# Kernel tuning notes

Hardware: AMD Instinct MI355X
Metric: run time of the kernel (lower is better)

## Reference

```python
import jax, jax.numpy as jnp
import numpy as np

B, H, W, C = 32, 64, 64, 256


def setup_inputs() -> dict:
    key = jax.random.key(0)
    ks = jax.random.split(key, 4)
    scale = 1.0 / np.sqrt(C)
    return {
        "x": jax.random.normal(ks[0], (B, H, W, C), dtype=jnp.float32),
        "wq": jax.random.normal(ks[1], (C, C), dtype=jnp.float32) * scale,
        "bq": jnp.zeros((C,), dtype=jnp.float32),
        "wk": jax.random.normal(ks[2], (C, C), dtype=jnp.float32) * scale,
        "bk": jnp.zeros((C,), dtype=jnp.float32),
        "wv": jax.random.normal(ks[3], (C, C), dtype=jnp.float32) * scale,
        "bv": jnp.zeros((C,), dtype=jnp.float32),
    }


def reference(x, wq, bq, wk, bk, wv, bv):
    # 1x1 convs == per-pixel dense projections
    q = jnp.einsum('bhwc,cf->bhwf', x, wq) + bq
    k = jnp.einsum('bhwc,cf->bhwf', x, wk) + bk
    v = jnp.einsum('bhwc,cf->bhwf', x, wv) + bv
    # tf.matmul(key, query, transpose_b=True): batch dims (b,h), contract over c
    attn = jnp.einsum('bhwc,bhvc->bhwv', k, q)  # [B,H,W,W], NO 1/sqrt(d) scaling
    attn = jax.nn.softmax(attn, axis=-1)
    out = jnp.einsum('bhwv,bhvc->bhwc', attn, v)  # [B,H,W,C]
    return out * x  # elementwise gate with raw input
```

## Files before the change

### kernel.cpp

```cpp
#include <hip/hip_runtime.h>

#define CD   256
#define WD   64
#define NBH  2048
#define XST  264
#define VST  72
#define SST  68

typedef unsigned short u16;
typedef __attribute__((ext_vector_type(8))) short bfrag_t;
typedef __attribute__((ext_vector_type(4))) float f4_t;

#define MFMA(a, b, c) __builtin_amdgcn_mfma_f32_16x16x32_bf16(a, b, c, 0, 0, 0)

__device__ __forceinline__ u16 f2bf(float f) {
    unsigned u = __float_as_uint(f);
    u += 0x7fffu + ((u >> 16) & 1u);
    return (u16)(u >> 16);
}
__device__ __forceinline__ float bf2f(u16 h) {
    return __uint_as_float(((unsigned)h) << 16);
}

__global__ __launch_bounds__(256) void prep_m(
    const float* __restrict__ wq, const float* __restrict__ wk,
    u16* __restrict__ Mthi, u16* __restrict__ Mtlo)
{
    __shared__ float swq[16 * 257];
    __shared__ float swk[32 * 257];
    const int t = threadIdx.x;
    const int dt = blockIdx.x >> 3;
    const int ct = blockIdx.x & 7;
    #pragma unroll
    for (int n = 0; n < 16; ++n) {
        int idx = n * 256 + t;
        int d = idx >> 8, f = idx & 255;
        swq[d * 257 + f] = wq[(dt * 16 + d) * CD + f];
    }
    #pragma unroll
    for (int n = 0; n < 32; ++n) {
        int idx = n * 256 + t;
        int c = idx >> 8, f = idx & 255;
        swk[c * 257 + f] = wk[(ct * 32 + c) * CD + f];
    }
    __syncthreads();
    const int d = t & 15, c0 = (t >> 4) * 2;
    #pragma unroll
    for (int cc = 0; cc < 2; ++cc) {
        const float* kr = &swk[(c0 + cc) * 257];
        const float* qr = &swq[d * 257];
        float acc = 0.f;
        #pragma unroll 8
        for (int f = 0; f < CD; ++f) acc = fmaf(kr[f], qr[f], acc);
        u16 h = f2bf(acc);
        int off = (dt * 16 + d) * CD + ct * 32 + c0 + cc;
        Mthi[off] = h;
        Mtlo[off] = f2bf(acc - bf2f(h));
    }
}

__global__ __launch_bounds__(256) void prep_v(
    const float* __restrict__ wv, u16* __restrict__ Wvthi)
{
    __shared__ float tile[64 * 65];
    const int t = threadIdx.x;
    const int bc = blockIdx.x >> 2, bd = blockIdx.x & 3;
    #pragma unroll
    for (int n = 0; n < 16; ++n) {
        int idx = n * 256 + t;
        int c = idx >> 6, d = idx & 63;
        tile[c * 65 + d] = wv[(bc * 64 + c) * CD + bd * 64 + d];
    }
    __syncthreads();
    #pragma unroll
    for (int n = 0; n < 16; ++n) {
        int idx = n * 256 + t;
        int d = idx >> 6, c = idx & 63;
        Wvthi[(bd * 64 + d) * CD + bc * 64 + c] = f2bf(tile[c * 65 + d]);
    }
}

__global__ __launch_bounds__(256) void prep_b(
    const float* __restrict__ wq, const float* __restrict__ bk,
    float* __restrict__ wqbk)
{
    __shared__ float sbk[CD];
    const int t = threadIdx.x;
    if (t < CD) sbk[t] = bk[t];
    __syncthreads();
    const int c = blockIdx.x * 16 + (t >> 4), part = t & 15;
    const float* wr = wq + c * CD + part * 16;
    const float* br = sbk + part * 16;
    float a = 0.f;
    #pragma unroll
    for (int j = 0; j < 16; ++j) a = fmaf(wr[j], br[j], a);
    a += __shfl_xor(a, 1);
    a += __shfl_xor(a, 2);
    a += __shfl_xor(a, 4);
    a += __shfl_xor(a, 8);
    if (part == 0) wqbk[c] = a;
}

extern __shared__ char smem_raw[];

__global__ __launch_bounds__(1024, 4) void attn_kernel(
    const float* __restrict__ x,
    const u16* __restrict__ Mthi, const u16* __restrict__ Mtlo,
    const u16* __restrict__ Wvthi, const float* __restrict__ wqbk,
    const float* __restrict__ bv, float* __restrict__ out)
{
    u16* sXhi = (u16*)smem_raw;
    u16* sXlo = sXhi + WD * XST;
    u16* sThi = sXlo + WD * XST;
    u16* sTlo = sThi + WD * XST;
    u16* sVt  = sThi;
    float* sS  = (float*)(sTlo + WD * XST);
    float* sxb = sS + WD * SST;
    float* sbv = sxb + WD;

    const int t = threadIdx.x;
    const int wave = t >> 6, lane = t & 63;
    const int lane15 = lane & 15, quad = lane >> 4;
    const int bh = blockIdx.x;
    const float* __restrict__ xblk = x + (size_t)bh * (WD * CD);
    float* __restrict__ oblk = out + (size_t)bh * (WD * CD);

    if (t < CD) sbv[t] = bv[t];
    {
        const float4* xv4 = (const float4*)xblk;
        #pragma unroll
        for (int n = 0; n < 4; ++n) {
            int idx = n * 1024 + t;
            float4 v = xv4[idx];
            int i = idx >> 6;
            int c = (idx & 63) << 2;
            ushort4 h4, l4;
            h4.x = f2bf(v.x); l4.x = f2bf(v.x - bf2f(h4.x));
            h4.y = f2bf(v.y); l4.y = f2bf(v.y - bf2f(h4.y));
            h4.z = f2bf(v.z); l4.z = f2bf(v.z - bf2f(h4.z));
            h4.w = f2bf(v.w); l4.w = f2bf(v.w - bf2f(h4.w));
            *(ushort4*)&sXhi[i * XST + c] = h4;
            *(ushort4*)&sXlo[i * XST + c] = l4;
        }
    }
    {
        const int row = t >> 4, part = t & 15;
        const float* xr = xblk + row * CD + part * 16;
        const float* br = wqbk + part * 16;
        float a = 0.f;
        #pragma unroll
        for (int i = 0; i < 4; ++i) {
            float4 xv = *(const float4*)&xr[i * 4];
            float4 bvv = *(const float4*)&br[i * 4];
            a = fmaf(xv.x, bvv.x, a); a = fmaf(xv.y, bvv.y, a);
            a = fmaf(xv.z, bvv.z, a); a = fmaf(xv.w, bvv.w, a);
        }
        a += __shfl_xor(a, 1);
        a += __shfl_xor(a, 2);
        a += __shfl_xor(a, 4);
        a += __shfl_xor(a, 8);
        if (part == 0) sxb[row] = a;
    }
    __syncthreads();

    {
        f4_t acc[4];
        const f4_t z = {0.f, 0.f, 0.f, 0.f};
        #pragma unroll
        for (int a = 0; a < 4; ++a) acc[a] = z;

        const int drow = wave * 16 + lane15;
        #pragma unroll
        for (int kk = 0; kk < 8; ++kk) {
            const int k0 = kk * 32 + quad * 8;
            const int mo = drow * CD + k0;
            bfrag_t Ah = *(const bfrag_t*)(Mthi + mo);
            bfrag_t Al = *(const bfrag_t*)(Mtlo + mo);
            bfrag_t Bh[4], Bl[4];
            #pragma unroll
            for (int nt = 0; nt < 4; ++nt) {
                const int xo = (nt * 16 + lane15) * XST + k0;
                Bh[nt] = *(const bfrag_t*)(sXhi + xo);
                Bl[nt] = *(const bfrag_t*)(sXlo + xo);
            }
            #pragma unroll
            for (int nt = 0; nt < 4; ++nt) {
                acc[nt] = MFMA(Ah, Bh[nt], acc[nt]);
                acc[nt] = MFMA(Ah, Bl[nt], acc[nt]);
                acc[nt] = MFMA(Al, Bh[nt], acc[nt]);
            }
        }
        #pragma unroll
        for (int nt = 0; nt < 4; ++nt) {
            const int i  = nt * 16 + lane15;
            const int d0 = wave * 16 + quad * 4;
            ushort4 h4, l4;
            float f;
            f = acc[nt][0]; h4.x = f2bf(f); l4.x = f2bf(f - bf2f(h4.x));
            f = acc[nt][1]; h4.y = f2bf(f); l4.y = f2bf(f - bf2f(h4.y));
            f = acc[nt][2]; h4.z = f2bf(f); l4.z = f2bf(f - bf2f(h4.z));
            f = acc[nt][3]; h4.w = f2bf(f); l4.w = f2bf(f - bf2f(h4.w));
            *(ushort4*)&sThi[i * XST + d0] = h4;
            *(ushort4*)&sTlo[i * XST + d0] = l4;
        }
    }
    __syncthreads();

    {
        f4_t acc = {0.f, 0.f, 0.f, 0.f};
        const int m0 = (wave >> 2) * 16;
        const int n0 = (wave & 3) * 16;
        #pragma unroll
        for (int kk = 0; kk < 8; ++kk) {
            const int k0 = kk * 32 + quad * 8;
            const int to = (m0 + lane15) * XST + k0;
            const int xo = (n0 + lane15) * XST + k0;
            bfrag_t Th = *(const bfrag_t*)(sThi + to);
            bfrag_t Tl = *(const bfrag_t*)(sTlo + to);
            bfrag_t Xh = *(const bfrag_t*)(sXhi + xo);
            bfrag_t Xl = *(const bfrag_t*)(sXlo + xo);
            acc = MFMA(Th, Xh, acc);
            acc = MFMA(Th, Xl, acc);
            acc = MFMA(Tl, Xh, acc);
        }
        const int v = n0 + lane15;
        const float xbv = sxb[v];
        #pragma unroll
        for (int r = 0; r < 4; ++r) {
            const int wtok = m0 + quad * 4 + r;
            sS[wtok * SST + v] = acc[r] + xbv;
        }
    }
    __syncthreads();

    {
        f4_t acc[4];
        const f4_t z = {0.f, 0.f, 0.f, 0.f};
        #pragma unroll
        for (int a = 0; a < 4; ++a) acc[a] = z;

        const int drow = wave * 16 + lane15;
        #pragma unroll
        for (int kk = 0; kk < 8; ++kk) {
            const int k0 = kk * 32 + quad * 8;
            bfrag_t Af = *(const bfrag_t*)(Wvthi + drow * CD + k0);
            #pragma unroll
            for (int nt = 0; nt < 4; ++nt) {
                bfrag_t Bf = *(const bfrag_t*)(sXhi + (nt * 16 + lane15) * XST + k0);
                acc[nt] = MFMA(Af, Bf, acc[nt]);
            }
        }
        #pragma unroll
        for (int nt = 0; nt < 4; ++nt) {
            const int j = nt * 16 + lane15;
            #pragma unroll
            for (int r = 0; r < 4; ++r) {
                const int d = wave * 16 + quad * 4 + r;
                sVt[d * VST + j] = f2bf(acc[nt][r] + sbv[d]);
            }
        }
    }
    {
        const int row = t >> 4, part = t & 15;
        float* srow = &sS[row * SST + part * 4];
        float e[4];
        float mx = fmaxf(fmaxf(srow[0], srow[1]), fmaxf(srow[2], srow[3]));
        mx = fmaxf(mx, __shfl_xor(mx, 1));
        mx = fmaxf(mx, __shfl_xor(mx, 2));
        mx = fmaxf(mx, __shfl_xor(mx, 4));
        mx = fmaxf(mx, __shfl_xor(mx, 8));
        float sum = 0.f;
        #pragma unroll
        for (int u = 0; u < 4; ++u) { e[u] = __expf(srow[u] - mx); sum += e[u]; }
        sum += __shfl_xor(sum, 1);
        sum += __shfl_xor(sum, 2);
        sum += __shfl_xor(sum, 4);
        sum += __shfl_xor(sum, 8);
        float inv = 1.0f / sum;
        #pragma unroll
        for (int u = 0; u < 4; ++u) srow[u] = e[u] * inv;
    }
    __syncthreads();

    {
        f4_t acc[4];
        const f4_t z = {0.f, 0.f, 0.f, 0.f};
        #pragma unroll
        for (int a = 0; a < 4; ++a) acc[a] = z;

        const int m0 = (wave & 3) * 16;
        const int nbase = (wave >> 2) * 64;
        #pragma unroll
        for (int kk = 0; kk < 2; ++kk) {
            const int k0 = kk * 32 + quad * 8;
            const float* p = &sS[(m0 + lane15) * SST + k0];
            f4_t p0 = *(const f4_t*)p;
            f4_t p1 = *(const f4_t*)(p + 4);
            bfrag_t Af;
            Af[0] = (short)f2bf(p0[0]); Af[1] = (short)f2bf(p0[1]);
            Af[2] = (short)f2bf(p0[2]); Af[3] = (short)f2bf(p0[3]);
            Af[4] = (short)f2bf(p1[0]); Af[5] = (short)f2bf(p1[1]);
            Af[6] = (short)f2bf(p1[2]); Af[7] = (short)f2bf(p1[3]);
            #pragma unroll
            for (int nt = 0; nt < 4; ++nt) {
                bfrag_t Bf = *(const bfrag_t*)(sVt + (nbase + nt * 16 + lane15) * VST + k0);
                acc[nt] = MFMA(Af, Bf, acc[nt]);
            }
        }
        #pragma unroll
        for (int nt = 0; nt < 4; ++nt) {
            const int d = nbase + nt * 16 + lane15;
            #pragma unroll
            for (int r = 0; r < 4; ++r) {
                const int wtok = m0 + quad * 4 + r;
                float g = xblk[wtok * CD + d];
                oblk[wtok * CD + d] = acc[nt][r] * g;
            }
        }
    }
}

extern "C" void kernel_launch(void* const* d_in, const int* in_sizes, int n_in,
                              void* d_out, int out_size, void* d_ws, size_t ws_size,
                              hipStream_t stream) {
    const float* x  = (const float*)d_in[0];
    const float* wq = (const float*)d_in[1];
    const float* wk = (const float*)d_in[3];
    const float* bk = (const float*)d_in[4];
    const float* wv = (const float*)d_in[5];
    const float* bv = (const float*)d_in[6];
    float* out = (float*)d_out;

    char* ws = (char*)d_ws;
    u16* Mthi   = (u16*)ws;
    u16* Mtlo   = (u16*)(ws + (128 << 10));
    u16* Wvthi  = (u16*)(ws + (256 << 10));
    float* wqbk = (float*)(ws + (384 << 10));

    prep_m<<<128, 256, 0, stream>>>(wq, wk, Mthi, Mtlo);
    prep_v<<<16, 256, 0, stream>>>(wv, Wvthi);
    prep_b<<<16, 256, 0, stream>>>(wq, bk, wqbk);

    const size_t lds = (size_t)(4 * WD * XST * sizeof(u16)) +
                       (WD * SST + WD + CD) * sizeof(float);
    hipFuncSetAttribute((const void*)attn_kernel,
                        hipFuncAttributeMaxDynamicSharedMemorySize, (int)lds);
    attn_kernel<<<NBH, 1024, lds, stream>>>(x, Mthi, Mtlo, Wvthi, wqbk, bv, out);
}
```

Before: 374.6 us.

## Merge prep kernels, preload weight fragments, split MFMA accumulator chains

Fuses the three weight-preparation kernels into one launch, with block index ranges selecting each task, to cut launch overhead. In the attention kernel, all global weight fragments (Mthi/Mtlo and Wvthi) are loaded into registers up front, so global latency is exposed once rather than inside the MFMA loop. The score GEMM now uses three independent accumulators instead of one serial chain of dependent MFMAs. Costs are higher register pressure under a 1024-thread launch bound and a slightly different float summation order.

Measured after the change: 374.3 us. Within noise of the previous version (-0.1%).

```diff
diff --git a/kernel.cpp b/kernel.cpp
--- a/kernel.cpp
+++ b/kernel.cpp
@@ -22,83 +22,80 @@
     return __uint_as_float(((unsigned)h) << 16);
 }
 
-__global__ __launch_bounds__(256) void prep_m(
+__global__ __launch_bounds__(256) void prep_all(
     const float* __restrict__ wq, const float* __restrict__ wk,
-    u16* __restrict__ Mthi, u16* __restrict__ Mtlo)
+    const float* __restrict__ wv, const float* __restrict__ bk,
+    u16* __restrict__ Mthi, u16* __restrict__ Mtlo,
+    u16* __restrict__ Wvthi, float* __restrict__ wqbk)
 {
-    __shared__ float swq[16 * 257];
-    __shared__ float swk[32 * 257];
+    __shared__ float smem[12336];
     const int t = threadIdx.x;
-    const int dt = blockIdx.x >> 3;
-    const int ct = blockIdx.x & 7;
-    #pragma unroll
-    for (int n = 0; n < 16; ++n) {
-        int idx = n * 256 + t;
-        int d = idx >> 8, f = idx & 255;
-        swq[d * 257 + f] = wq[(dt * 16 + d) * CD + f];
-    }
-    #pragma unroll
-    for (int n = 0; n < 32; ++n) {
-        int idx = n * 256 + t;
-        int c = idx >> 8, f = idx & 255;
-        swk[c * 257 + f] = wk[(ct * 32 + c) * CD + f];
-    }
-    __syncthreads();
-    const int d = t & 15, c0 = (t >> 4) * 2;
-    #pragma unroll
-    for (int cc = 0; cc < 2; ++cc) {
-        const float* kr = &swk[(c0 + cc) * 257];
-        const float* qr = &swq[d * 257];
-        float acc = 0.f;
-        #pragma unroll 8
-        for (int f = 0; f < CD; ++f) acc = fmaf(kr[f], qr[f], acc);
-        u16 h = f2bf(acc);
-        int off = (dt * 16 + d) * CD + ct * 32 + c0 + cc;
-        Mthi[off] = h;
-        Mtlo[off] = f2bf(acc - bf2f(h));
-    }
-}
-
-__global__ __launch_bounds__(256) void prep_v(
-    const float* __restrict__ wv, u16* __restrict__ Wvthi)
-{
-    __shared__ float tile[64 * 65];
-    const int t = threadIdx.x;
-    const int bc = blockIdx.x >> 2, bd = blockIdx.x & 3;
-    #pragma unroll
-    for (int n = 0; n < 16; ++n) {
-        int idx = n * 256 + t;
-        int c = idx >> 6, d = idx & 63;
-        tile[c * 65 + d] = wv[(bc * 64 + c) * CD + bd * 64 + d];
-    }
-    __syncthreads();
-    #pragma unroll
-    for (int n = 0; n < 16; ++n) {
-        int idx = n * 256 + t;
-        int d = idx >> 6, c = idx & 63;
-        Wvthi[(bd * 64 + d) * CD + bc * 64 + c] = f2bf(tile[c * 65 + d]);
-    }
-}
-
-__global__ __launch_bounds__(256) void prep_b(
-    const float* __restrict__ wq, const float* __restrict__ bk,
-    float* __restrict__ wqbk)
-{
-    __shared__ float sbk[CD];
-    const int t = threadIdx.x;
-    if (t < CD) sbk[t] = bk[t];
-    __syncthreads();
-    const int c = blockIdx.x * 16 + (t >> 4), part = t & 15;
-    const float* wr = wq + c * CD + part * 16;
-    const float* br = sbk + part * 16;
-    float a = 0.f;
-    #pragma unroll
-    for (int j = 0; j < 16; ++j) a = fmaf(wr[j], br[j], a);
-    a += __shfl_xor(a, 1);
-    a += __shfl_xor(a, 2);
-    a += __shfl_xor(a, 4);
-    a += __shfl_xor(a, 8);
-    if (part == 0) wqbk[c] = a;
+    const int b = blockIdx.x;
+
+    if (b < 128) {
+        float* swq = smem;
+        float* swk = smem + 16 * 257;
+        const int dt = b >> 3;
+        const int ct = b & 7;
+        #pragma unroll
+        for (int n = 0; n < 16; ++n) {
+            int idx = n * 256 + t;
+            int d = idx >> 8, f = idx & 255;
+            swq[d * 257 + f] = wq[(dt * 16 + d) * CD + f];
+        }
+        #pragma unroll
+        for (int n = 0; n < 32; ++n) {
+            int idx = n * 256 + t;
+            int c = idx >> 8, f = idx & 255;
+            swk[c * 257 + f] = wk[(ct * 32 + c) * CD + f];
+        }
+        __syncthreads();
+        const int d = t & 15, c0 = (t >> 4) * 2;
+        #pragma unroll
+        for (int cc = 0; cc < 2; ++cc) {
+            const float* kr = &swk[(c0 + cc) * 257];
+            const float* qr = &swq[d * 257];
+            float acc = 0.f;
+            #pragma unroll 8
+            for (int f = 0; f < CD; ++f) acc = fmaf(kr[f], qr[f], acc);
+            u16 h = f2bf(acc);
+            int off = (dt * 16 + d) * CD + ct * 32 + c0 + cc;
+            Mthi[off] = h;
+            Mtlo[off] = f2bf(acc - bf2f(h));
+        }
+    } else if (b < 144) {
+        float* tile = smem;
+        const int bb = b - 128;
+        const int bc = bb >> 2, bd = bb & 3;
+        #pragma unroll
+        for (int n = 0; n < 16; ++n) {
+            int idx = n * 256 + t;
+            int c = idx >> 6, d = idx & 63;
+            tile[c * 65 + d] = wv[(bc * 64 + c) * CD + bd * 64 + d];
+        }
+        __syncthreads();
+        #pragma unroll
+        for (int n = 0; n < 16; ++n) {
+            int idx = n * 256 + t;
+            int d = idx >> 6, c = idx & 63;
+            Wvthi[(bd * 64 + d) * CD + bc * 64 + c] = f2bf(tile[c * 65 + d]);
+        }
+    } else {
+        float* sbk = smem;
+        if (t < CD) sbk[t] = bk[t];
+        __syncthreads();
+        const int c = (b - 144) * 16 + (t >> 4), part = t & 15;
+        const float* wr = wq + c * CD + part * 16;
+        const float* br = sbk + part * 16;
+        float a = 0.f;
+        #pragma unroll
+        for (int j = 0; j < 16; ++j) a = fmaf(wr[j], br[j], a);
+        a += __shfl_xor(a, 1);
+        a += __shfl_xor(a, 2);
+        a += __shfl_xor(a, 4);
+        a += __shfl_xor(a, 8);
+        if (part == 0) wqbk[c] = a;
+    }
 }
 
 extern __shared__ char smem_raw[];
@@ -170,12 +167,17 @@
         for (int a = 0; a < 4; ++a) acc[a] = z;
 
         const int drow = wave * 16 + lane15;
+        const u16* mh = Mthi + drow * CD + quad * 8;
+        const u16* ml = Mtlo + drow * CD + quad * 8;
+        bfrag_t Ah[8], Al[8];
+        #pragma unroll
+        for (int kk = 0; kk < 8; ++kk) {
+            Ah[kk] = *(const bfrag_t*)(mh + kk * 32);
+            Al[kk] = *(const bfrag_t*)(ml + kk * 32);
+        }
         #pragma unroll
         for (int kk = 0; kk < 8; ++kk) {
             const int k0 = kk * 32 + quad * 8;
-            const int mo = drow * CD + k0;
-            bfrag_t Ah = *(const bfrag_t*)(Mthi + mo);
-            bfrag_t Al = *(const bfrag_t*)(Mtlo + mo);
             bfrag_t Bh[4], Bl[4];
             #pragma unroll
             for (int nt = 0; nt < 4; ++nt) {
@@ -185,9 +187,9 @@
             }
             #pragma unroll
             for (int nt = 0; nt < 4; ++nt) {
-                acc[nt] = MFMA(Ah, Bh[nt], acc[nt]);
-                acc[nt] = MFMA(Ah, Bl[nt], acc[nt]);
-                acc[nt] = MFMA(Al, Bh[nt], acc[nt]);
+                acc[nt] = MFMA(Ah[kk], Bh[nt], acc[nt]);
+                acc[nt] = MFMA(Ah[kk], Bl[nt], acc[nt]);
+                acc[nt] = MFMA(Al[kk], Bh[nt], acc[nt]);
             }
         }
         #pragma unroll
@@ -207,7 +209,8 @@
     __syncthreads();
 
     {
-        f4_t acc = {0.f, 0.f, 0.f, 0.f};
+        const f4_t z = {0.f, 0.f, 0.f, 0.f};
+        f4_t a0 = z, a1 = z, a2 = z;
         const int m0 = (wave >> 2) * 16;
         const int n0 = (wave & 3) * 16;
         #pragma unroll
@@ -219,16 +222,16 @@
             bfrag_t Tl = *(const bfrag_t*)(sTlo + to);
             bfrag_t Xh = *(const bfrag_t*)(sXhi + xo);
             bfrag_t Xl = *(const bfrag_t*)(sXlo + xo);
-            acc = MFMA(Th, Xh, acc);
-            acc = MFMA(Th, Xl, acc);
-            acc = MFMA(Tl, Xh, acc);
+            a0 = MFMA(Th, Xh, a0);
+            a1 = MFMA(Th, Xl, a1);
+            a2 = MFMA(Tl, Xh, a2);
         }
         const int v = n0 + lane15;
         const float xbv = sxb[v];
         #pragma unroll
         for (int r = 0; r < 4; ++r) {
             const int wtok = m0 + quad * 4 + r;
-            sS[wtok * SST + v] = acc[r] + xbv;
+            sS[wtok * SST + v] = a0[r] + a1[r] + a2[r] + xbv;
         }
     }
     __syncthreads();
@@ -240,14 +243,18 @@
         for (int a = 0; a < 4; ++a) acc[a] = z;
 
         const int drow = wave * 16 + lane15;
+        const u16* wvp = Wvthi + drow * CD + quad * 8;
+        bfrag_t Av[8];
+        #pragma unroll
+        for (int kk = 0; kk < 8; ++kk)
+            Av[kk] = *(const bfrag_t*)(wvp + kk * 32);
         #pragma unroll
         for (int kk = 0; kk < 8; ++kk) {
             const int k0 = kk * 32 + quad * 8;
-            bfrag_t Af = *(const bfrag_t*)(Wvthi + drow * CD + k0);
             #pragma unroll
             for (int nt = 0; nt < 4; ++nt) {
                 bfrag_t Bf = *(const bfrag_t*)(sXhi + (nt * 16 + lane15) * XST + k0);
-                acc[nt] = MFMA(Af, Bf, acc[nt]);
+                acc[nt] = MFMA(Av[kk], Bf, acc[nt]);
             }
         }
         #pragma unroll
@@ -337,9 +344,7 @@
     u16* Wvthi  = (u16*)(ws + (256 << 10));
     float* wqbk = (float*)(ws + (384 << 10));
 
-    prep_m<<<128, 256, 0, stream>>>(wq, wk, Mthi, Mtlo);
-    prep_v<<<16, 256, 0, stream>>>(wv, Wvthi);
-    prep_b<<<16, 256, 0, stream>>>(wq, bk, wqbk);
+    prep_all<<<160, 256, 0, stream>>>(wq, wk, wv, bk, Mthi, Mtlo, Wvthi, wqbk);
 
     const size_t lds = (size_t)(4 * WD * XST * sizeof(u16)) +
                        (WD * SST + WD + CD) * sizeof(float);
```
